# Optimization experiments

Measured on AMD Instinct MI355X. Metric: run time of the kernel, lower is better.

## Reference

```python
import jax, jax.numpy as jnp
import numpy as np

B_SZ = 4; SEQ = 2048; D_INPUT = 40; D_MODEL = 128; N_LAYERS = 4
D_STATE = 16; EXPAND = 2; D_INNER = D_MODEL * EXPAND
N_HEADS = 4; D_HEAD = D_MODEL // N_HEADS; MAX_LANDMARKS = 100
EPS_RMS = 1.1920929e-07  # torch nn.RMSNorm default eps = finfo(float32).eps
EPS_LN = 1e-5
A_FLOOR = 1e-4


def _rms(x, w):
    return x * jax.lax.rsqrt(jnp.mean(x * x, -1, keepdims=True) + EPS_RMS) * w


def _ln(x, w, b):
    m = jnp.mean(x, -1, keepdims=True)
    v = jnp.mean((x - m) ** 2, -1, keepdims=True)
    return (x - m) * jax.lax.rsqrt(v + EPS_LN) * w + b


def _mamba3_block(xin, Wi, Wx, Wdt, bdt, Alog, Bb, Cb, Bnw, Cnw, rf, Dv, Wo):
    # xin: (B,L,d_model)
    xz = xin @ Wi                       # (B,L,2*d_inner)
    xp, z = jnp.split(xz, 2, axis=-1)
    xp = jax.nn.silu(xp)
    sp = xp @ Wx                        # (B,L,2*d_state+2)
    B_raw = sp[..., :D_STATE]
    C_raw = sp[..., D_STATE:2 * D_STATE]
    dt_in = sp[..., -2:-1]
    lam_in = sp[..., -1:]
    Bm = _rms(B_raw + Bb, Bnw)
    Cm = _rms(C_raw + Cb, Cnw)
    dt = jax.nn.softplus(dt_in @ Wdt + bdt)   # (B,L,d_inner)
    lam = jax.nn.sigmoid(lam_in)              # (B,L,1)
    # data-dependent RoPE on B and C
    freqs = jax.nn.softplus(rf)                                  # (d_state//2,)
    ang = jnp.cumsum(jnp.mean(dt, -1, keepdims=True), axis=1) * freqs  # (B,L,ds/2)
    ca, sa = jnp.cos(ang), jnp.sin(ang)

    def rot(M):
        e, o = M[..., ::2], M[..., 1::2]
        return jnp.stack([e * ca - o * sa, e * sa + o * ca], -1).reshape(M.shape)

    Bm, Cm = rot(Bm), rot(Cm)
    A = jnp.minimum(-jnp.exp(Alog), -A_FLOOR)   # (d_inner,d_state)
    dte = dt[..., None]                          # (B,L,d_inner,1)
    dA = jnp.exp(A * dte)                        # (B,L,d_inner,d_state)
    Bx = Bm[:, :, None, :] * xp[..., None]       # (B,L,d_inner,d_state)
    Bx_prev = jnp.concatenate([jnp.zeros_like(Bx[:, :1]), Bx[:, :-1]], axis=1)
    lame = lam[..., None]                        # (B,L,1,1)
    u = (1.0 - lame) * dte * dA * Bx_prev + lame * dte * Bx
    u = u.at[:, 0].set(dte[:, 0] * Bx[:, 0])     # t==0 case: h = dt*B*x (no lambda)

    def step(h, inp):
        dA_t, u_t, C_t = inp
        h = dA_t * h + u_t
        return h, jnp.sum(h * C_t[:, None, :], -1)

    h0 = jnp.zeros((xin.shape[0], D_INNER, D_STATE), xin.dtype)
    _, ys = jax.lax.scan(step, h0, (jnp.swapaxes(dA, 0, 1), jnp.swapaxes(u, 0, 1), jnp.swapaxes(Cm, 0, 1)))
    y = jnp.swapaxes(ys, 0, 1)                   # (B,L,d_inner)
    y = y + xp * Dv
    y = y * jax.nn.silu(z)
    return y @ Wo


def _landmark_attn(mo, skip, hw, WQ, bQ, WK, bK, WV, bV, WO, bO):
    Bsz, L, Dm = skip.shape
    k = min(MAX_LANDMARKS, L)
    _, idx = jax.lax.top_k(hw, k)
    idx = jnp.sort(idx, axis=1)                            # (B,k)
    kv = jnp.take_along_axis(skip, idx[..., None], axis=1)  # (B,k,Dm)
    q = mo[:, -1:, :]                                       # (B,1,Dm)
    Q = (q @ WQ + bQ).reshape(Bsz, 1, N_HEADS, D_HEAD).transpose(0, 2, 1, 3)
    K = (kv @ WK + bK).reshape(Bsz, k, N_HEADS, D_HEAD).transpose(0, 2, 1, 3)
    V = (kv @ WV + bV).reshape(Bsz, k, N_HEADS, D_HEAD).transpose(0, 2, 1, 3)
    scores = jnp.einsum('bhqd,bhkd->bhqk', Q, K) * (D_HEAD ** -0.5)
    probs = jax.nn.softmax(scores, axis=-1)
    out = jnp.einsum('bhqk,bhkd->bhqd', probs, V).transpose(0, 2, 1, 3).reshape(Bsz, Dm)
    return out @ WO + bO


def setup_inputs() -> dict:
    key = jax.random.key(0)
    ks = iter(jax.random.split(key, 64))

    def nrm(shape, s=0.02):
        return jax.random.normal(next(ks), shape, jnp.float32) * s

    nl, ds, di, dm = N_LAYERS, D_STATE, D_INNER, D_MODEL
    inp = {}
    inp['x'] = jax.random.normal(next(ks), (B_SZ, SEQ, D_INPUT), jnp.float32)
    inp['hawkes_weights'] = jax.random.uniform(next(ks), (B_SZ, SEQ), jnp.float32)
    inp['emb_W'] = nrm((D_INPUT, dm)); inp['emb_b'] = jnp.zeros(dm, jnp.float32)
    inp['skip_W'] = nrm((D_INPUT, dm)); inp['skip_b'] = jnp.zeros(dm, jnp.float32)
    inp['in_proj_W'] = nrm((nl, dm, 2 * di))
    inp['x_proj_W'] = nrm((nl, di, 2 * ds + 2))
    inp['dt_proj_W'] = nrm((nl, 1, di), 1.0)
    inp['dt_proj_b'] = jnp.full((nl, di), -1.0, jnp.float32)
    inp['A_log'] = jnp.broadcast_to(jnp.log(jnp.arange(1, ds + 1, dtype=jnp.float32)), (nl, di, ds)) * jnp.ones((nl, di, ds), jnp.float32)
    inp['B_bias'] = jnp.ones((nl, ds), jnp.float32)
    inp['C_bias'] = jnp.ones((nl, ds), jnp.float32)
    inp['Bn_w'] = jnp.ones((nl, ds), jnp.float32)
    inp['Cn_w'] = jnp.ones((nl, ds), jnp.float32)
    inp['rope_freqs'] = nrm((nl, ds // 2), 0.01)
    inp['D_param'] = jnp.ones((nl, di), jnp.float32)
    inp['out_proj_W'] = nrm((nl, di, dm))
    inp['ln_w'] = jnp.ones((nl, dm), jnp.float32); inp['ln_b'] = jnp.zeros((nl, dm), jnp.float32)
    inp['fn_w'] = jnp.ones(dm, jnp.float32); inp['fn_b'] = jnp.zeros(dm, jnp.float32)
    for nm in ('Q', 'K', 'V', 'O'):
        inp['W' + nm] = nrm((dm, dm)); inp['b' + nm] = jnp.zeros(dm, jnp.float32)
    return inp


def reference(x, hawkes_weights, emb_W, emb_b, skip_W, skip_b, in_proj_W, x_proj_W,
              dt_proj_W, dt_proj_b, A_log, B_bias, C_bias, Bn_w, Cn_w, rope_freqs,
              D_param, out_proj_W, ln_w, ln_b, fn_w, fn_b, WQ, bQ, WK, bK, WV, bV, WO, bO):
    w = hawkes_weights[..., None]
    h = (x @ emb_W + emb_b) * w          # Hawkes-damped embedding for Mamba path
    skip = (x @ skip_W + skip_b) * w     # Hawkes skip for attention KV
    for i in range(N_LAYERS):
        h = h + _mamba3_block(_ln(h, ln_w[i], ln_b[i]), in_proj_W[i], x_proj_W[i],
                              dt_proj_W[i], dt_proj_b[i], A_log[i], B_bias[i], C_bias[i],
                              Bn_w[i], Cn_w[i], rope_freqs[i], D_param[i], out_proj_W[i])
    mo = _ln(h, fn_w, fn_b)
    return _landmark_attn(mo, skip, hawkes_weights, WQ, bQ, WK, bK, WV, bV, WO, bO)
```

## Files before the change

### kernel.cpp

```cpp
#include <hip/hip_runtime.h>
#include <hip/hip_fp16.h>
#include <math.h>

#define BSZ   4
#define SEQL  2048
#define DIN   40
#define DM    128
#define DI    256
#define DS    16
#define NL    4
#define NHEAD 4
#define DHEAD 32
#define KLM   100
#define NC    128
#define TC    16
#define NROWS 8
#define EROWS 16

__device__ __forceinline__ float rcp_(float x){ return __builtin_amdgcn_rcpf(x); }
__device__ __forceinline__ float sigmoidf_(float x){ return rcp_(1.0f + __expf(-x)); }
__device__ __forceinline__ float siluf_(float x){ return x*rcp_(1.0f + __expf(-x)); }
__device__ __forceinline__ float softplusf_(float x){ return fmaxf(x,0.0f) + __logf(1.0f + __expf(-fabsf(x))); }

__device__ __forceinline__ void load8(const float* p, float* r){
  const float4* q = (const float4*)p;
  float4 a=q[0], b=q[1];
  r[0]=a.x;r[1]=a.y;r[2]=a.z;r[3]=a.w; r[4]=b.x;r[5]=b.y;r[6]=b.z;r[7]=b.w;
}
__device__ __forceinline__ void store8(float* p, const float* r){
  float4* q = (float4*)p;
  q[0]=make_float4(r[0],r[1],r[2],r[3]);  q[1]=make_float4(r[4],r[5],r[6],r[7]);
}
__device__ __forceinline__ void load16(const float* p, float* r){
  load8(p, r); load8(p+8, r+8);
}
__device__ __forceinline__ void store16(float* p, const float* r){
  store8(p, r); store8(p+8, r+8);
}

__global__ __launch_bounds__(256) void topk_kernel(
    const float* __restrict__ hw, int* __restrict__ idxl_g)
{
  __shared__ int redcnt[2][4];
  __shared__ int eqc[8][4], gtc[8][4];

  const int b = blockIdx.x;
  const int t = threadIdx.x;
  const int lane = t & 63, w = t >> 6;

  const float* hwp = hw + (size_t)b*SEQL;
  unsigned vb[8];
  #pragma unroll
  for (int q=0;q<8;q++) vb[q] = __float_as_uint(hwp[q*256 + t]);

  unsigned kth = 0u;
  for (int bit=31; bit>=0; --bit){
    const unsigned cand = kth | (1u << bit);
    int c0 = 0;
    #pragma unroll
    for (int q=0;q<8;q++) c0 += __popcll(__ballot(vb[q] >= cand));
    const int par = bit & 1;
    if (lane == 0) redcnt[par][w] = c0;
    __syncthreads();
    const int tot = redcnt[par][0]+redcnt[par][1]+redcnt[par][2]+redcnt[par][3];
    if (tot >= KLM) kth = cand;
  }

  unsigned long long beq[8], bgt[8];
  #pragma unroll
  for (int q=0;q<8;q++){
    beq[q] = __ballot(vb[q] == kth);
    bgt[q] = __ballot(vb[q] >  kth);
  }
  if (lane == 0){
    #pragma unroll
    for (int q=0;q<8;q++){ eqc[q][w] = __popcll(beq[q]); gtc[q][w] = __popcll(bgt[q]); }
  }
  __syncthreads();
  {
    int gtTot = 0;
    #pragma unroll
    for (int q=0;q<8;q++) gtTot += gtc[q][0]+gtc[q][1]+gtc[q][2]+gtc[q][3];
    const int need_eq = KLM - gtTot;
    const unsigned long long lmask = (lane==0) ? 0ull : ((~0ull) >> (64-lane));
    int eqPfx = 0, gtPfx = 0;
    #pragma unroll
    for (int q=0;q<8;q++){
      int eqWP = 0, gtWP = 0;
      for (int w2=0; w2<w; ++w2){ eqWP += eqc[q][w2]; gtWP += gtc[q][w2]; }
      const int eqBefore = eqPfx + eqWP + __popcll(beq[q] & lmask);
      const int gtBefore = gtPfx + gtWP + __popcll(bgt[q] & lmask);
      if (vb[q] > kth){
        const int pos = gtBefore + min(eqBefore, need_eq);
        if (pos < KLM) idxl_g[b*KLM + pos] = q*256 + t;
      } else if (vb[q] == kth && eqBefore < need_eq){
        const int pos = gtBefore + eqBefore;
        if (pos < KLM) idxl_g[b*KLM + pos] = q*256 + t;
      }
      eqPfx += eqc[q][0]+eqc[q][1]+eqc[q][2]+eqc[q][3];
      gtPfx += gtc[q][0]+gtc[q][1]+gtc[q][2]+gtc[q][3];
    }
  }
}

__global__ __launch_bounds__(256) void embed_kernel(
    const float* __restrict__ x, const float* __restrict__ hw,
    const float* __restrict__ eW, const float* __restrict__ eb,
    const float* __restrict__ sW, const float* __restrict__ sb,
    float* __restrict__ hb, float* __restrict__ sk)
{
  __shared__ float xr[EROWS][DIN];
  const int t = threadIdx.x;
  const size_t R0 = (size_t)blockIdx.x * EROWS;
  for (int e=t; e<EROWS*DIN; e+=256) ((float*)xr)[e] = x[R0*DIN + e];
  __syncthreads();
  const int c = t & (DM-1), g = t >> 7;
  float ae[8], as[8];
  #pragma unroll
  for (int j=0;j<8;j++){ ae[j]=0.0f; as[j]=0.0f; }
  for (int k=0;k<DIN;k++){
    const float we  = eW[(size_t)k*DM + c];
    const float ws_ = sW[(size_t)k*DM + c];
    #pragma unroll
    for (int j=0;j<8;j++){
      const float xv = xr[g*8+j][k];
      ae[j] = fmaf(xv, we, ae[j]);
      as[j] = fmaf(xv, ws_, as[j]);
    }
  }
  const float ebv = eb[c], sbv = sb[c];
  #pragma unroll
  for (int j=0;j<8;j++){
    const size_t R = R0 + g*8 + j;
    const float w = hw[R];
    hb[R*DM + c] = (ae[j]+ebv)*w;
    sk[R*DM + c] = (as[j]+sbv)*w;
  }
}

__global__ __launch_bounds__(256) void pre_kernel(
    const float* __restrict__ hb,
    const float* __restrict__ Wi, const float* __restrict__ Wx,
    const float* __restrict__ Wdt, const float* __restrict__ bdt,
    const float* __restrict__ Bb, const float* __restrict__ Cb,
    const float* __restrict__ Bnw, const float* __restrict__ Cnw,
    const float* __restrict__ lnw, const float* __restrict__ lnb,
    __half* __restrict__ xph, __half* __restrict__ zsh,
    float* __restrict__ dtin, float* __restrict__ Shalf,
    float* __restrict__ Bmb, float* __restrict__ Cmb,
    float* __restrict__ lamb, float* __restrict__ mdtb)
{
  __shared__ float xin[NROWS][DM+4];
  __shared__ float xps[NROWS][DI+4];
  __shared__ float spl[NROWS][40];
  __shared__ float pr[NROWS][4];

  const int t = threadIdx.x;
  const size_t R0 = (size_t)blockIdx.x * NROWS;

  {
    const int r = t >> 5, j = t & 31;
    const float4 v = ((const float4*)(hb + (R0 + r)*DM))[j];
    float s = v.x+v.y+v.z+v.w;
    #pragma unroll
    for (int o=16;o>0;o>>=1) s += __shfl_xor(s,o,32);
    const float m = s*(1.0f/DM);
    const float dx=v.x-m, dy=v.y-m, dz=v.z-m, dw=v.w-m;
    float ss = dx*dx+dy*dy+dz*dz+dw*dw;
    #pragma unroll
    for (int o=16;o>0;o>>=1) ss += __shfl_xor(ss,o,32);
    const float inv = 1.0f/sqrtf(ss*(1.0f/DM) + 1e-5f);
    const int c = j*4;
    xin[r][c+0] = dx*inv*lnw[c+0] + lnb[c+0];
    xin[r][c+1] = dy*inv*lnw[c+1] + lnb[c+1];
    xin[r][c+2] = dz*inv*lnw[c+2] + lnb[c+2];
    xin[r][c+3] = dw*inv*lnw[c+3] + lnb[c+3];
  }
  __syncthreads();

  {
    float2 a[NROWS];
    #pragma unroll
    for (int r=0;r<NROWS;r++){ a[r].x=0.0f; a[r].y=0.0f; }
    for (int k=0;k<DM;k+=4){
      const float2 w0 = *(const float2*)&Wi[(size_t)(k+0)*(2*DI) + 2*t];
      const float2 w1 = *(const float2*)&Wi[(size_t)(k+1)*(2*DI) + 2*t];
      const float2 w2 = *(const float2*)&Wi[(size_t)(k+2)*(2*DI) + 2*t];
      const float2 w3 = *(const float2*)&Wi[(size_t)(k+3)*(2*DI) + 2*t];
      #pragma unroll
      for (int r=0;r<NROWS;r++){
        const float4 xv = *(const float4*)&xin[r][k];
        a[r].x = fmaf(xv.x,w0.x,a[r].x); a[r].y = fmaf(xv.x,w0.y,a[r].y);
        a[r].x = fmaf(xv.y,w1.x,a[r].x); a[r].y = fmaf(xv.y,w1.y,a[r].y);
        a[r].x = fmaf(xv.z,w2.x,a[r].x); a[r].y = fmaf(xv.z,w2.y,a[r].y);
        a[r].x = fmaf(xv.w,w3.x,a[r].x); a[r].y = fmaf(xv.w,w3.y,a[r].y);
      }
    }
    if (t < 128){
      #pragma unroll
      for (int r=0;r<NROWS;r++){
        const float sx = siluf_(a[r].x), sy = siluf_(a[r].y);
        xps[r][2*t] = sx; xps[r][2*t+1] = sy;
        *(__half2*)&xph[(R0+r)*DI + 2*t] =
            __halves2half2(__float2half_rn(sx), __float2half_rn(sy));
      }
    } else {
      const int zc = 2*t - 2*DI + DI;
      #pragma unroll
      for (int r=0;r<NROWS;r++){
        const float sx = siluf_(a[r].x), sy = siluf_(a[r].y);
        *(__half2*)&zsh[(R0+r)*DI + zc] =
            __halves2half2(__float2half_rn(sx), __float2half_rn(sy));
      }
    }
  }
  __syncthreads();

  if (t < 136){
    const int r = t & 7, op = t >> 3;
    float ax=0.0f, ay=0.0f;
    for (int k=0;k<DI;k+=4){
      const float4 xv = *(const float4*)&xps[r][k];
      const float2 w0 = *(const float2*)&Wx[(size_t)(k+0)*34 + 2*op];
      const float2 w1 = *(const float2*)&Wx[(size_t)(k+1)*34 + 2*op];
      const float2 w2 = *(const float2*)&Wx[(size_t)(k+2)*34 + 2*op];
      const float2 w3 = *(const float2*)&Wx[(size_t)(k+3)*34 + 2*op];
      ax = fmaf(xv.x,w0.x,ax); ay = fmaf(xv.x,w0.y,ay);
      ax = fmaf(xv.y,w1.x,ax); ay = fmaf(xv.y,w1.y,ay);
      ax = fmaf(xv.z,w2.x,ax); ay = fmaf(xv.z,w2.y,ay);
      ax = fmaf(xv.w,w3.x,ax); ay = fmaf(xv.w,w3.y,ay);
    }
    spl[r][2*op] = ax; spl[r][2*op+1] = ay;
  }
  __syncthreads();

  {
    const int half = t >> 7;
    const int r2 = (t >> 4) & 7, s2 = t & 15;
    const float* bias = half ? Cb : Bb;
    const float* wn   = half ? Cnw : Bnw;
    const float v = spl[r2][half*DS + s2] + bias[s2];
    float ss = v*v;
    #pragma unroll
    for (int o=8;o>0;o>>=1) ss += __shfl_xor(ss,o,16);
    const float inv = 1.0f/sqrtf(ss*(1.0f/DS) + 1.1920929e-07f);
    (half ? Cmb : Bmb)[(R0+r2)*DS + s2] = v*inv*wn[s2];
  }

  {
    const int lane = t & 63, w = t >> 6;
    const float wdt = Wdt[t], bdtv = bdt[t];
    float Sd = 0.0f;
    #pragma unroll
    for (int r=0;r<NROWS;r++){
      const float dval = softplusf_(fmaf(spl[r][32], wdt, bdtv));
      Sd += dval;
      float s = dval;
      #pragma unroll
      for (int o=32;o>0;o>>=1) s += __shfl_xor(s,o,64);
      if (lane==0) pr[r][w] = s;
    }
    Shalf[(size_t)blockIdx.x * DI + t] = Sd;
    if (t < NROWS){
      lamb[R0+t] = sigmoidf_(spl[t][33]);
      dtin[R0+t] = spl[t][32];
    }
  }
  __syncthreads();
  if (t < NROWS)
    mdtb[R0+t] = (pr[t][0]+pr[t][1]+pr[t][2]+pr[t][3])*(1.0f/DI);
}

__global__ __launch_bounds__(256) void cumsum_kernel(
    const float* __restrict__ mdt, double* __restrict__ csum_g)
{
  __shared__ double wsum[4];
  const int b = blockIdx.x, t = threadIdx.x;
  const int lane = t & 63, w = t >> 6;
  const float* p = mdt + (size_t)b*SEQL + (size_t)t*8;
  double v[8]; double s = 0.0;
  #pragma unroll
  for (int q=0;q<8;q++){ v[q] = (double)p[q]; s += v[q]; }
  double sc = s;
  #pragma unroll
  for (int o=1;o<64;o<<=1){
    const double nb = __shfl_up(sc, o, 64);
    if (lane >= o) sc += nb;
  }
  if (lane==63) wsum[w] = sc;
  __syncthreads();
  double woff = 0.0;
  for (int j=0;j<w;j++) woff += wsum[j];
  double run = woff + sc - s;
  double* dst = csum_g + (size_t)b*SEQL + (size_t)t*8;
  #pragma unroll
  for (int q=0;q<8;q++){ run += v[q]; dst[q] = run; }
}

__global__ __launch_bounds__(256) void csfill_kernel(
    const double* __restrict__ csum_g, const float* __restrict__ rf,
    float2* __restrict__ cst)
{
  __shared__ double fqs[8];
  const int t = threadIdx.x;
  if (t < 8){
    const double xfr = (double)rf[t];
    fqs[t] = fmax(xfr, 0.0) + log1p(exp(-fabs(xfr)));
  }
  __syncthreads();
  const int row = blockIdx.x*256 + t;
  const double ab = csum_g[row];
  const double TWO_PI = 6.283185307179586;
  const double INV2PI = 0.15915494309189535;
  float2 o8[8];
  #pragma unroll
  for (int f=0; f<8; f++){
    const double ang = ab * fqs[f];
    const double red = ang - floor(ang*INV2PI)*TWO_PI;
    float sa, ca;
    __sincosf((float)red, &sa, &ca);
    o8[f] = make_float2(ca, sa);
  }
  float4* dst = (float4*)&cst[(size_t)row*8];
  dst[0] = make_float4(o8[0].x,o8[0].y,o8[1].x,o8[1].y);
  dst[1] = make_float4(o8[2].x,o8[2].y,o8[3].x,o8[3].y);
  dst[2] = make_float4(o8[4].x,o8[4].y,o8[5].x,o8[5].y);
  dst[3] = make_float4(o8[6].x,o8[6].y,o8[7].x,o8[7].y);
}

__global__ __launch_bounds__(512) void scan1_kernel(
    const __half* __restrict__ xph, const float* __restrict__ dtin,
    const float* __restrict__ Wdt, const float* __restrict__ bdt,
    const float* __restrict__ Bmb, const float* __restrict__ lamb,
    const float2* __restrict__ cst,
    const float* __restrict__ Alog, float* __restrict__ hend)
{
  __shared__ float Bst[TC+1][DS];
  __shared__ float lst[TC];
  __shared__ float dsl[TC];
  __shared__ __half xpl[TC+1][DI+8];
  const int t = threadIdx.x;
  const int d  = t >> 1;
  const int s0 = (t & 1) * 8;
  const int c = blockIdx.x & (NC-1);
  const int b = blockIdx.x >> 7;
  const size_t bL = (size_t)b*SEQL;
  const int t0 = c*TC;
  const int id = blockIdx.x*256 + d;

  for (int e=t; e<(TC+1)*DS; e+=512){
    const int j = e >> 4, s = e & 15;
    const int trow = t0 - 1 + j;
    Bst[j][s] = (trow >= 0) ? Bmb[(bL + trow)*DS + s] : 0.0f;
  }
  for (int e=t; e<(TC+1)*DI; e+=512){
    const int j = e >> 8, dd = e & (DI-1);
    const int trow = t0 - 1 + j;
    xpl[j][dd] = (trow >= 0) ? xph[(bL + trow)*DI + dd] : __float2half_rn(0.0f);
  }
  if (t < TC){
    lst[t] = lamb[bL + t0 + t];
    dsl[t] = dtin[bL + t0 + t];
  }
  __syncthreads();
  if (t < 136){
    const int j = t >> 3, f = t & 7;
    const int trow = t0 - 1 + j;
    if (trow >= 0){
      const float2 cs = cst[((size_t)(bL + trow))*8 + f];
      const float e0 = Bst[j][2*f], o0 = Bst[j][2*f+1];
      Bst[j][2*f]   = e0*cs.x - o0*cs.y;
      Bst[j][2*f+1] = e0*cs.y + o0*cs.x;
    }
  }
  __syncthreads();

  float A[8];
  #pragma unroll
  for (int s=0;s<8;s++) A[s] = fminf(-__expf(Alog[d*DS + s0 + s]), -1e-4f);
  const float wdt = Wdt[d], bdtv = bdt[d];
  float h[8], Bprev[8];
  #pragma unroll
  for (int s=0;s<8;s++) h[s]=0.0f;
  float xpm1;
  int tstart;
  if (t0 > 0){
    #pragma unroll
    for (int s=0;s<8;s++) Bprev[s] = Bst[0][s0+s];
    xpm1 = __half2float(xpl[0][d]);
    tstart = 0;
  } else {
    const float dtv = softplusf_(fmaf(dsl[0], wdt, bdtv));
    const float xpv = __half2float(xpl[1][d]);
    #pragma unroll
    for (int s=0;s<8;s++){
      h[s] = dtv*(Bst[1][s0+s]*xpv);
      Bprev[s] = Bst[1][s0+s];
    }
    xpm1 = xpv;
    tstart = 1;
  }
  for (int j=tstart; j<TC; ++j){
    const float dtv = softplusf_(fmaf(dsl[j], wdt, bdtv));
    const float xpv = __half2float(xpl[j+1][d]);
    const float lamv = lst[j];
    const float dl = dtv*lamv;
    const float dml = dtv - dl;
    #pragma unroll
    for (int s=0;s<8;s++){
      const float a = __expf(A[s]*dtv);
      const float Bc = Bst[j+1][s0+s];
      const float u = fmaf(dml*a, Bprev[s]*xpm1, dl*(Bc*xpv));
      h[s] = fmaf(a, h[s], u);
      Bprev[s] = Bc;
    }
    xpm1 = xpv;
  }
  store8(hend + (size_t)id*DS + s0, h);
}

__global__ __launch_bounds__(128) void scan2_kernel(
    float* __restrict__ hend, const float* __restrict__ Shalf,
    const float* __restrict__ Alog)
{
  __shared__ float hS[NC][DS+1];
  __shared__ float pS[NC][DS+1];
  const int c = threadIdx.x;
  const int d = blockIdx.x & (DI-1);
  const int b = blockIdx.x >> 8;
  const float S = Shalf[(size_t)(b*(SEQL/NROWS) + 2*c)*DI + d]
                + Shalf[(size_t)(b*(SEQL/NROWS) + 2*c + 1)*DI + d];
  float P[DS], h[DS];
  #pragma unroll
  for (int s=0;s<DS;s++){
    const float A = fminf(-__expf(Alog[d*DS+s]), -1e-4f);
    P[s] = __expf(A*S);
  }
  load16(hend + (((size_t)(b*NC + c))*DI + d)*DS, h);
  #pragma unroll
  for (int s=0;s<DS;s++){ hS[c][s]=h[s]; pS[c][s]=P[s]; }
  __syncthreads();
  for (int off=1; off<NC; off<<=1){
    float hn[DS], pn[DS];
    const int src = c - off;
    if (src >= 0){
      #pragma unroll
      for (int s=0;s<DS;s++){ hn[s]=hS[src][s]; pn[s]=pS[src][s]; }
    }
    __syncthreads();
    if (src >= 0){
      #pragma unroll
      for (int s=0;s<DS;s++){
        h[s] = fmaf(P[s], hn[s], h[s]);
        P[s] *= pn[s];
        hS[c][s] = h[s]; pS[c][s] = P[s];
      }
    }
    __syncthreads();
  }
  float o[DS];
  if (c == 0){
    #pragma unroll
    for (int s=0;s<DS;s++) o[s] = 0.0f;
  } else {
    #pragma unroll
    for (int s=0;s<DS;s++) o[s] = hS[c-1][s];
  }
  store16(hend + (((size_t)(b*NC + c))*DI + d)*DS, o);
}

__global__ __launch_bounds__(512) void scan3post_kernel(
    const __half* __restrict__ xph, const float* __restrict__ dtin,
    const float* __restrict__ Wdt, const float* __restrict__ bdt,
    const float* __restrict__ Bmb, const float* __restrict__ Cmb,
    const float* __restrict__ lamb, const __half* __restrict__ zsh,
    const float2* __restrict__ cst,
    const float* __restrict__ Alog, const float* __restrict__ Dv,
    const float* __restrict__ Hin, const float* __restrict__ Wo,
    float* __restrict__ hb)
{
  __shared__ float Bst[TC+1][DS];
  __shared__ float Cst[TC][DS];
  __shared__ float lst[TC];
  __shared__ float dsl[TC];
  __shared__ __half xpl[TC+1][DI+8];
  __shared__ __half zsl[TC][DI+8];
  __shared__ float ys[TC][DI+4];
  const int t = threadIdx.x;
  const int d  = t >> 1;
  const int sh = t & 1;
  const int s0 = sh * 8;
  const int c = blockIdx.x & (NC-1);
  const int b = blockIdx.x >> 7;
  const size_t bL = (size_t)b*SEQL;
  const int t0 = c*TC;
  const int id = blockIdx.x*256 + d;

  for (int e=t; e<(TC+1)*DS; e+=512){
    const int j = e >> 4, s = e & 15;
    const int trow = t0 - 1 + j;
    Bst[j][s] = (trow >= 0) ? Bmb[(bL + trow)*DS + s] : 0.0f;
    if (j < TC) Cst[j][s] = Cmb[(bL + t0 + j)*DS + s];
  }
  for (int e=t; e<(TC+1)*DI; e+=512){
    const int j = e >> 8, dd = e & (DI-1);
    const int trow = t0 - 1 + j;
    xpl[j][dd] = (trow >= 0) ? xph[(bL + trow)*DI + dd] : __float2half_rn(0.0f);
    if (j < TC) zsl[j][dd] = zsh[(bL + t0 + j)*DI + dd];
  }
  if (t < TC){
    lst[t] = lamb[bL + t0 + t];
    dsl[t] = dtin[bL + t0 + t];
  }
  __syncthreads();
  if (t < 264){
    if (t < 136){
      const int j = t >> 3, f = t & 7;
      const int trow = t0 - 1 + j;
      if (trow >= 0){
        const float2 cs = cst[((size_t)(bL + trow))*8 + f];
        const float e0 = Bst[j][2*f], o0 = Bst[j][2*f+1];
        Bst[j][2*f]   = e0*cs.x - o0*cs.y;
        Bst[j][2*f+1] = e0*cs.y + o0*cs.x;
      }
    } else {
      const int e2 = t - 136;
      const int j = e2 >> 3, f = e2 & 7;
      const float2 cs = cst[((size_t)(bL + t0 + j))*8 + f];
      const float e0 = Cst[j][2*f], o0 = Cst[j][2*f+1];
      Cst[j][2*f]   = e0*cs.x - o0*cs.y;
      Cst[j][2*f+1] = e0*cs.y + o0*cs.x;
    }
  }
  __syncthreads();

  float A[8];
  #pragma unroll
  for (int s=0;s<8;s++) A[s] = fminf(-__expf(Alog[d*DS + s0 + s]), -1e-4f);
  const float wdt = Wdt[d], bdtv = bdt[d];
  const float dvp = Dv[d];
  float h[8], Bprev[8];
  load8(Hin + (size_t)id*DS + s0, h);
  float xpm1;
  int tstart;
  if (t0 > 0){
    #pragma unroll
    for (int s=0;s<8;s++) Bprev[s] = Bst[0][s0+s];
    xpm1 = __half2float(xpl[0][d]);
    tstart = 0;
  } else {
    const float dtv = softplusf_(fmaf(dsl[0], wdt, bdtv));
    const float xpv = __half2float(xpl[1][d]);
    float y = 0.0f;
    #pragma unroll
    for (int s=0;s<8;s++){
      h[s] = dtv*(Bst[1][s0+s]*xpv);
      y = fmaf(h[s], Cst[0][s0+s], y);
      Bprev[s] = Bst[1][s0+s];
    }
    const float ytot = y + __shfl_xor(y, 1, 64);
    if (sh == 0) ys[0][d] = (ytot + xpv*dvp)*__half2float(zsl[0][d]);
    xpm1 = xpv;
    tstart = 1;
  }
  for (int j=tstart; j<TC; ++j){
    const float dtv = softplusf_(fmaf(dsl[j], wdt, bdtv));
    const float xpv = __half2float(xpl[j+1][d]);
    const float lamv = lst[j];
    const float dl = dtv*lamv;
    const float dml = dtv - dl;
    float y = 0.0f;
    #pragma unroll
    for (int s=0;s<8;s++){
      const float a = __expf(A[s]*dtv);
      const float Bc = Bst[j+1][s0+s];
      const float u = fmaf(dml*a, Bprev[s]*xpm1, dl*(Bc*xpv));
      h[s] = fmaf(a, h[s], u);
      y = fmaf(h[s], Cst[j][s0+s], y);
      Bprev[s] = Bc;
    }
    const float ytot = y + __shfl_xor(y, 1, 64);
    if (sh == 0) ys[j][d] = (ytot + xpv*dvp)*__half2float(zsl[j][d]);
    xpm1 = xpv;
  }
  __syncthreads();

  {
    const int cg2  = t & 31;
    const int ks2  = (t >> 5) & 1;
    const int rg   = (t >> 6) & 3;
    const int ksHi = t >> 8;
    const int seg = ksHi*2 + ks2;
    const int k0 = seg*64;
    const int c0c = cg2*4;
    float acc[4][4];
    #pragma unroll
    for (int rr=0;rr<4;rr++){ acc[rr][0]=0.f; acc[rr][1]=0.f; acc[rr][2]=0.f; acc[rr][3]=0.f; }
    for (int k=k0; k<k0+64; k+=4){
      float4 yv[4];
      #pragma unroll
      for (int rr=0;rr<4;rr++) yv[rr] = *(const float4*)&ys[rg*4+rr][k];
      #pragma unroll
      for (int j=0;j<4;j++){
        const float4 wv = *(const float4*)&Wo[(size_t)(k+j)*DM + c0c];
        const float y0 = (j==0)?yv[0].x:(j==1)?yv[0].y:(j==2)?yv[0].z:yv[0].w;
        const float y1 = (j==0)?yv[1].x:(j==1)?yv[1].y:(j==2)?yv[1].z:yv[1].w;
        const float y2 = (j==0)?yv[2].x:(j==1)?yv[2].y:(j==2)?yv[2].z:yv[2].w;
        const float y3 = (j==0)?yv[3].x:(j==1)?yv[3].y:(j==2)?yv[3].z:yv[3].w;
        acc[0][0]=fmaf(y0,wv.x,acc[0][0]); acc[0][1]=fmaf(y0,wv.y,acc[0][1]);
        acc[0][2]=fmaf(y0,wv.z,acc[0][2]); acc[0][3]=fmaf(y0,wv.w,acc[0][3]);
        acc[1][0]=fmaf(y1,wv.x,acc[1][0]); acc[1][1]=fmaf(y1,wv.y,acc[1][1]);
        acc[1][2]=fmaf(y1,wv.z,acc[1][2]); acc[1][3]=fmaf(y1,wv.w,acc[1][3]);
        acc[2][0]=fmaf(y2,wv.x,acc[2][0]); acc[2][1]=fmaf(y2,wv.y,acc[2][1]);
        acc[2][2]=fmaf(y2,wv.z,acc[2][2]); acc[2][3]=fmaf(y2,wv.w,acc[2][3]);
        acc[3][0]=fmaf(y3,wv.x,acc[3][0]); acc[3][1]=fmaf(y3,wv.y,acc[3][1]);
        acc[3][2]=fmaf(y3,wv.z,acc[3][2]); acc[3][3]=fmaf(y3,wv.w,acc[3][3]);
      }
    }
    #pragma unroll
    for (int rr=0;rr<4;rr++){
      #pragma unroll
      for (int cc=0;cc<4;cc++) acc[rr][cc] += __shfl_down(acc[rr][cc], 32, 64);
    }
    float (*red)[132] = (float(*)[132])ys;
    __syncthreads();
    const int lane = t & 63;
    if (ksHi == 1 && lane < 32){
      #pragma unroll
      for (int rr=0;rr<4;rr++)
        *(float4*)&red[rg*4+rr][c0c] = make_float4(acc[rr][0],acc[rr][1],acc[rr][2],acc[rr][3]);
    }
    __syncthreads();
    if (ksHi == 0 && lane < 32){
      #pragma unroll
      for (int rr=0;rr<4;rr++){
        const float4 rv = *(const float4*)&red[rg*4+rr][c0c];
        const size_t row = bL + t0 + rg*4 + rr;
        float4 hv = *(const float4*)&hb[row*DM + c0c];
        hv.x += acc[rr][0] + rv.x; hv.y += acc[rr][1] + rv.y;
        hv.z += acc[rr][2] + rv.z; hv.w += acc[rr][3] + rv.w;
        *(float4*)&hb[row*DM + c0c] = hv;
      }
    }
  }
}

__global__ __launch_bounds__(256) void attnmid_kernel(
    const float* __restrict__ hb, const float* __restrict__ sk,
    const int* __restrict__ idxl_g,
    const float* __restrict__ fnw, const float* __restrict__ fnb,
    const float* __restrict__ WQ, const float* __restrict__ bQ,
    const float* __restrict__ WK, const float* __restrict__ bK,
    const float* __restrict__ WV, const float* __restrict__ bV,
    float* __restrict__ attnog)
{
  __shared__ float kv[KLM][DM+4];
  __shared__ float mo[DM];
  __shared__ float Qs[DHEAD];
  __shared__ float qk[DM];
  __shared__ float sc[KLM];
  __shared__ float pbar[DM];
  __shared__ float bterm_s;
  const int t = threadIdx.x;
  const int b = blockIdx.x >> 2, hh = blockIdx.x & 3;
  const int c0 = hh*DHEAD;

  if (t < 64){
    const float* hr = hb + ((size_t)b*SEQL + (SEQL-1))*DM;
    const float v0 = hr[t], v1 = hr[t+64];
    float s = v0+v1;
    #pragma unroll
    for (int o=32;o>0;o>>=1) s += __shfl_xor(s,o,64);
    const float m = s*(1.0f/DM);
    const float d0=v0-m, d1=v1-m;
    float ss = d0*d0 + d1*d1;
    #pragma unroll
    for (int o=32;o>0;o>>=1) ss += __shfl_xor(ss,o,64);
    const float inv = 1.0f/sqrtf(ss*(1.0f/DM) + 1e-5f);
    mo[t]    = d0*inv*fnw[t]    + fnb[t];
    mo[t+64] = d1*inv*fnw[t+64] + fnb[t+64];
  }
  for (int e=t; e<KLM*DM; e+=256){
    const int j = e >> 7, cc = e & (DM-1);
    kv[j][cc] = sk[((size_t)b*SEQL + idxl_g[b*KLM + j])*DM + cc];
  }
  __syncthreads();
  if (t < DHEAD){
    float a = bQ[c0+t];
    #pragma unroll 4
    for (int k=0;k<DM;k++) a = fmaf(mo[k], WQ[(size_t)k*DM + c0+t], a);
    Qs[t] = a;
  }
  __syncthreads();
  if (t < DM){
    float a = 0.0f;
    #pragma unroll
    for (int cc=0; cc<DHEAD; cc++) a = fmaf(WK[(size_t)t*DM + c0 + cc], Qs[cc], a);
    qk[t] = a;
  } else if (t == DM){
    float a = 0.0f;
    for (int cc=0; cc<DHEAD; cc++) a += bK[c0+cc]*Qs[cc];
    bterm_s = a;
  }
  __syncthreads();
  if (t < KLM){
    float a = bterm_s;
    for (int m=0;m<DM;m+=4){
      const float4 kvv = *(const float4*)&kv[t][m];
      const float4 qv  = *(const float4*)&qk[m];
      a = fmaf(kvv.x,qv.x,a); a = fmaf(kvv.y,qv.y,a);
      a = fmaf(kvv.z,qv.z,a); a = fmaf(kvv.w,qv.w,a);
    }
    sc[t] = a*0.17677669529663687f;
  }
  __syncthreads();
  if (t < 64){
    const int lane = t;
    const float v0 = (lane < KLM) ? sc[lane] : -3.0e38f;
    const float v1 = (lane+64 < KLM) ? sc[lane+64] : -3.0e38f;
    float mx = fmaxf(v0, v1);
    #pragma unroll
    for (int o2=32;o2>0;o2>>=1) mx = fmaxf(mx, __shfl_xor(mx,o2,64));
    const float e0 = (lane < KLM) ? __expf(v0-mx) : 0.0f;
    const float e1 = (lane+64 < KLM) ? __expf(v1-mx) : 0.0f;
    float sm = e0+e1;
    #pragma unroll
    for (int o2=32;o2>0;o2>>=1) sm += __shfl_xor(sm,o2,64);
    const float inv2 = rcp_(sm);
    if (lane < KLM) sc[lane] = e0*inv2;
    if (lane+64 < KLM) sc[lane+64] = e1*inv2;
  }
  __syncthreads();
  if (t < DM){
    float a = 0.0f;
    #pragma unroll 4
    for (int j=0;j<KLM;j++) a = fmaf(sc[j], kv[j][t], a);
    pbar[t] = a;
  }
  __syncthreads();
  if (t < DHEAD){
    const int cc = c0 + t;
    float a = bV[cc];
    #pragma unroll 4
    for (int m=0;m<DM;m++) a = fmaf(pbar[m], WV[(size_t)m*DM + cc], a);
    attnog[b*DM + cc] = a;
  }
}

__global__ __launch_bounds__(128) void attnout_kernel(
    const float* __restrict__ attnog, const float* __restrict__ WO,
    const float* __restrict__ bO, float* __restrict__ outp)
{
  __shared__ float ao[DM];
  const int b = blockIdx.x, t = threadIdx.x;
  ao[t] = attnog[b*DM + t];
  __syncthreads();
  float a = bO[t];
  #pragma unroll 4
  for (int c2=0;c2<DM;c2++) a = fmaf(ao[c2], WO[(size_t)c2*DM + t], a);
  outp[(size_t)b*DM + t] = a;
}

extern "C" void kernel_launch(void* const* d_in, const int* in_sizes, int n_in,
                              void* d_out, int out_size, void* d_ws, size_t ws_size,
                              hipStream_t stream)
{
  (void)in_sizes; (void)n_in; (void)out_size; (void)ws_size;
  const float* x    = (const float*)d_in[0];
  const float* hw   = (const float*)d_in[1];
  const float* embW = (const float*)d_in[2];
  const float* embB = (const float*)d_in[3];
  const float* skW  = (const float*)d_in[4];
  const float* skB  = (const float*)d_in[5];
  const float* inW  = (const float*)d_in[6];
  const float* xpW  = (const float*)d_in[7];
  const float* dtW  = (const float*)d_in[8];
  const float* dtB  = (const float*)d_in[9];
  const float* Alog = (const float*)d_in[10];
  const float* Bb   = (const float*)d_in[11];
  const float* Cb   = (const float*)d_in[12];
  const float* Bnw  = (const float*)d_in[13];
  const float* Cnw  = (const float*)d_in[14];
  const float* rf   = (const float*)d_in[15];
  const float* Dpar = (const float*)d_in[16];
  const float* outW = (const float*)d_in[17];
  const float* lnW  = (const float*)d_in[18];
  const float* lnB  = (const float*)d_in[19];
  const float* fnW  = (const float*)d_in[20];
  const float* fnB  = (const float*)d_in[21];
  const float* WQ = (const float*)d_in[22]; const float* bQ = (const float*)d_in[23];
  const float* WK = (const float*)d_in[24]; const float* bK = (const float*)d_in[25];
  const float* WV = (const float*)d_in[26]; const float* bV = (const float*)d_in[27];
  const float* WO = (const float*)d_in[28]; const float* bO = (const float*)d_in[29];

  float* ws = (float*)d_ws;
  size_t off = 0;
  float* hb    = ws + off; off += (size_t)BSZ*SEQL*DM;
  float* sk    = ws + off; off += (size_t)BSZ*SEQL*DM;
  __half* xph  = (__half*)(ws + off); off += (size_t)BSZ*SEQL*DI/2;
  __half* zsh  = (__half*)(ws + off); off += (size_t)BSZ*SEQL*DI/2;
  float* Bmb   = ws + off; off += (size_t)BSZ*SEQL*DS;
  float* Cmb   = ws + off; off += (size_t)BSZ*SEQL*DS;
  float* lamb  = ws + off; off += (size_t)BSZ*SEQL;
  float* mdtb  = ws + off; off += (size_t)BSZ*SEQL;
  float* dtin  = ws + off; off += (size_t)BSZ*SEQL;
  float* Shalf = ws + off; off += (size_t)BSZ*(SEQL/NROWS)*DI;
  float* hend  = ws + off; off += (size_t)BSZ*NC*DI*DS;
  float2* cst  = (float2*)(ws + off); off += (size_t)BSZ*SEQL*16;
  double* csum_g = (double*)(ws + off); off += (size_t)BSZ*SEQL*2;
  int* idxl_g  = (int*)(ws + off); off += (size_t)BSZ*KLM;
  float* attnog= ws + off; off += (size_t)BSZ*DM;

  topk_kernel<<<BSZ, 256, 0, stream>>>(hw, idxl_g);
  embed_kernel<<<BSZ*SEQL/EROWS, 256, 0, stream>>>(x, hw, embW, embB, skW, skB, hb, sk);

  for (int i=0;i<NL;i++){
    pre_kernel<<<BSZ*SEQL/NROWS, 256, 0, stream>>>(hb,
        inW + (size_t)i*DM*2*DI, xpW + (size_t)i*DI*34,
        dtW + (size_t)i*DI, dtB + (size_t)i*DI,
        Bb + i*DS, Cb + i*DS, Bnw + i*DS, Cnw + i*DS,
        lnW + i*DM, lnB + i*DM,
        xph, zsh, dtin, Shalf, Bmb, Cmb, lamb, mdtb);
    cumsum_kernel<<<BSZ, 256, 0, stream>>>(mdtb, csum_g);
    csfill_kernel<<<BSZ*SEQL/256, 256, 0, stream>>>(csum_g, rf + i*8, cst);
    scan1_kernel<<<BSZ*NC, 512, 0, stream>>>(xph, dtin,
        dtW + (size_t)i*DI, dtB + (size_t)i*DI,
        Bmb, lamb, cst, Alog + (size_t)i*DI*DS, hend);
    scan2_kernel<<<BSZ*DI, 128, 0, stream>>>(hend, Shalf, Alog + (size_t)i*DI*DS);
    scan3post_kernel<<<BSZ*NC, 512, 0, stream>>>(xph, dtin,
        dtW + (size_t)i*DI, dtB + (size_t)i*DI,
        Bmb, Cmb, lamb, zsh, cst,
        Alog + (size_t)i*DI*DS, Dpar + (size_t)i*DI, hend,
        outW + (size_t)i*DI*DM, hb);
  }

  attnmid_kernel<<<BSZ*NHEAD, 256, 0, stream>>>(hb, sk, idxl_g, fnW, fnB,
      WQ, bQ, WK, bK, WV, bV, attnog);
  attnout_kernel<<<BSZ, 128, 0, stream>>>(attnog, WO, bO, (float*)d_out);
}
```

Baseline: 506.7 us.

## Split pre and scan kernels across d_inner halves and add residual kernel

The pre kernel is launched with twice the blocks: each block computes either the x or the z half of the input projection, and the z blocks exit early. The scan1 and scan3post kernels split d_inner into two halves per chunk, with four threads per channel holding four states each. Each half writes a partial output projection to a new buffer, and a new resid_kernel adds both partials into the hidden state. The aim is more blocks, lower register pressure and better occupancy. In exchange it adds an extra kernel launch per layer, extra global traffic for the partial outputs, and a duplicated layernorm per row block in pre.

```diff
diff --git a/kernel.cpp b/kernel.cpp
--- a/kernel.cpp
+++ b/kernel.cpp
@@ -22,20 +22,18 @@
 __device__ __forceinline__ float siluf_(float x){ return x*rcp_(1.0f + __expf(-x)); }
 __device__ __forceinline__ float softplusf_(float x){ return fmaxf(x,0.0f) + __logf(1.0f + __expf(-fabsf(x))); }
 
-__device__ __forceinline__ void load8(const float* p, float* r){
-  const float4* q = (const float4*)p;
-  float4 a=q[0], b=q[1];
-  r[0]=a.x;r[1]=a.y;r[2]=a.z;r[3]=a.w; r[4]=b.x;r[5]=b.y;r[6]=b.z;r[7]=b.w;
-}
-__device__ __forceinline__ void store8(float* p, const float* r){
-  float4* q = (float4*)p;
-  q[0]=make_float4(r[0],r[1],r[2],r[3]);  q[1]=make_float4(r[4],r[5],r[6],r[7]);
+__device__ __forceinline__ void load4(const float* p, float* r){
+  const float4 a = *(const float4*)p;
+  r[0]=a.x; r[1]=a.y; r[2]=a.z; r[3]=a.w;
+}
+__device__ __forceinline__ void store4(float* p, const float* r){
+  *(float4*)p = make_float4(r[0],r[1],r[2],r[3]);
 }
 __device__ __forceinline__ void load16(const float* p, float* r){
-  load8(p, r); load8(p+8, r+8);
+  load4(p,r); load4(p+4,r+4); load4(p+8,r+8); load4(p+12,r+12);
 }
 __device__ __forceinline__ void store16(float* p, const float* r){
-  store8(p, r); store8(p+8, r+8);
+  store4(p,r); store4(p+4,r+4); store4(p+8,r+8); store4(p+12,r+12);
 }
 
 __global__ __launch_bounds__(256) void topk_kernel(
@@ -156,7 +154,9 @@
   __shared__ float pr[NROWS][4];
 
   const int t = threadIdx.x;
-  const size_t R0 = (size_t)blockIdx.x * NROWS;
+  const int rb = blockIdx.x >> 1;
+  const int typeB = blockIdx.x & 1;
+  const size_t R0 = (size_t)rb * NROWS;
 
   {
     const int r = t >> 5, j = t & 31;
@@ -179,39 +179,36 @@
   __syncthreads();
 
   {
-    float2 a[NROWS];
-    #pragma unroll
-    for (int r=0;r<NROWS;r++){ a[r].x=0.0f; a[r].y=0.0f; }
+    const int col = typeB*DI + t;
+    float acc[NROWS];
+    #pragma unroll
+    for (int r=0;r<NROWS;r++) acc[r] = 0.0f;
+    const float* Wc = Wi + col;
     for (int k=0;k<DM;k+=4){
-      const float2 w0 = *(const float2*)&Wi[(size_t)(k+0)*(2*DI) + 2*t];
-      const float2 w1 = *(const float2*)&Wi[(size_t)(k+1)*(2*DI) + 2*t];
-      const float2 w2 = *(const float2*)&Wi[(size_t)(k+2)*(2*DI) + 2*t];
-      const float2 w3 = *(const float2*)&Wi[(size_t)(k+3)*(2*DI) + 2*t];
+      const float w0 = Wc[(size_t)(k+0)*(2*DI)];
+      const float w1 = Wc[(size_t)(k+1)*(2*DI)];
+      const float w2 = Wc[(size_t)(k+2)*(2*DI)];
+      const float w3 = Wc[(size_t)(k+3)*(2*DI)];
       #pragma unroll
       for (int r=0;r<NROWS;r++){
         const float4 xv = *(const float4*)&xin[r][k];
-        a[r].x = fmaf(xv.x,w0.x,a[r].x); a[r].y = fmaf(xv.x,w0.y,a[r].y);
-        a[r].x = fmaf(xv.y,w1.x,a[r].x); a[r].y = fmaf(xv.y,w1.y,a[r].y);
-        a[r].x = fmaf(xv.z,w2.x,a[r].x); a[r].y = fmaf(xv.z,w2.y,a[r].y);
-        a[r].x = fmaf(xv.w,w3.x,a[r].x); a[r].y = fmaf(xv.w,w3.y,a[r].y);
+        float a = acc[r];
+        a = fmaf(xv.x,w0,a); a = fmaf(xv.y,w1,a);
+        a = fmaf(xv.z,w2,a); a = fmaf(xv.w,w3,a);
+        acc[r] = a;
       }
     }
-    if (t < 128){
+    if (typeB){
       #pragma unroll
-      for (int r=0;r<NROWS;r++){
-        const float sx = siluf_(a[r].x), sy = siluf_(a[r].y);
-        xps[r][2*t] = sx; xps[r][2*t+1] = sy;
-        *(__half2*)&xph[(R0+r)*DI + 2*t] =
-            __halves2half2(__float2half_rn(sx), __float2half_rn(sy));
-      }
-    } else {
-      const int zc = 2*t - 2*DI + DI;
-      #pragma unroll
-      for (int r=0;r<NROWS;r++){
-        const float sx = siluf_(a[r].x), sy = siluf_(a[r].y);
-        *(__half2*)&zsh[(R0+r)*DI + zc] =
-            __halves2half2(__float2half_rn(sx), __float2half_rn(sy));
-      }
+      for (int r=0;r<NROWS;r++)
+        zsh[(R0+r)*DI + t] = __float2half_rn(siluf_(acc[r]));
+      return;
+    }
+    #pragma unroll
+    for (int r=0;r<NROWS;r++){
+      const float sx = siluf_(acc[r]);
+      xps[r][t] = sx;
+      xph[(R0+r)*DI + t] = __float2half_rn(sx);
     }
   }
   __syncthreads();
@@ -260,7 +257,7 @@
       for (int o=32;o>0;o>>=1) s += __shfl_xor(s,o,64);
       if (lane==0) pr[r][w] = s;
     }
-    Shalf[(size_t)blockIdx.x * DI + t] = Sd;
+    Shalf[(size_t)rb * DI + t] = Sd;
     if (t < NROWS){
       lamb[R0+t] = sigmoidf_(spl[t][33]);
       dtin[R0+t] = spl[t][32];
@@ -338,25 +335,27 @@
   __shared__ float Bst[TC+1][DS];
   __shared__ float lst[TC];
   __shared__ float dsl[TC];
-  __shared__ __half xpl[TC+1][DI+8];
+  __shared__ __half xpl[TC+1][128+8];
   const int t = threadIdx.x;
-  const int d  = t >> 1;
-  const int s0 = (t & 1) * 8;
-  const int c = blockIdx.x & (NC-1);
-  const int b = blockIdx.x >> 7;
+  const int half = blockIdx.x & 1;
+  const int c = (blockIdx.x >> 1) & (NC-1);
+  const int b = blockIdx.x >> 8;
+  const int dl = t >> 2;
+  const int d  = half*128 + dl;
+  const int s0 = (t & 3)*4;
   const size_t bL = (size_t)b*SEQL;
   const int t0 = c*TC;
-  const int id = blockIdx.x*256 + d;
-
-  for (int e=t; e<(TC+1)*DS; e+=512){
-    const int j = e >> 4, s = e & 15;
+  const size_t idg = ((size_t)(b*NC + c))*DI + d;
+
+  if (t < 272){
+    const int j = t >> 4, s = t & 15;
     const int trow = t0 - 1 + j;
     Bst[j][s] = (trow >= 0) ? Bmb[(bL + trow)*DS + s] : 0.0f;
   }
-  for (int e=t; e<(TC+1)*DI; e+=512){
-    const int j = e >> 8, dd = e & (DI-1);
+  for (int e=t; e<(TC+1)*128; e+=512){
+    const int j = e >> 7, dd = e & 127;
     const int trow = t0 - 1 + j;
-    xpl[j][dd] = (trow >= 0) ? xph[(bL + trow)*DI + dd] : __float2half_rn(0.0f);
+    xpl[j][dd] = (trow >= 0) ? xph[(bL + trow)*DI + half*128 + dd] : __float2half_rn(0.0f);
   }
   if (t < TC){
     lst[t] = lamb[bL + t0 + t];
@@ -375,25 +374,25 @@
   }
   __syncthreads();
 
-  float A[8];
-  #pragma unroll
-  for (int s=0;s<8;s++) A[s] = fminf(-__expf(Alog[d*DS + s0 + s]), -1e-4f);
+  float A[4];
+  #pragma unroll
+  for (int s=0;s<4;s++) A[s] = fminf(-__expf(Alog[d*DS + s0 + s]), -1e-4f);
   const float wdt = Wdt[d], bdtv = bdt[d];
-  float h[8], Bprev[8];
-  #pragma unroll
-  for (int s=0;s<8;s++) h[s]=0.0f;
+  float h[4], Bprev[4];
+  #pragma unroll
+  for (int s=0;s<4;s++) h[s]=0.0f;
   float xpm1;
   int tstart;
   if (t0 > 0){
     #pragma unroll
-    for (int s=0;s<8;s++) Bprev[s] = Bst[0][s0+s];
-    xpm1 = __half2float(xpl[0][d]);
+    for (int s=0;s<4;s++) Bprev[s] = Bst[0][s0+s];
+    xpm1 = __half2float(xpl[0][dl]);
     tstart = 0;
   } else {
     const float dtv = softplusf_(fmaf(dsl[0], wdt, bdtv));
-    const float xpv = __half2float(xpl[1][d]);
-    #pragma unroll
-    for (int s=0;s<8;s++){
+    const float xpv = __half2float(xpl[1][dl]);
+    #pragma unroll
+    for (int s=0;s<4;s++){
       h[s] = dtv*(Bst[1][s0+s]*xpv);
       Bprev[s] = Bst[1][s0+s];
     }
@@ -402,21 +401,21 @@
   }
   for (int j=tstart; j<TC; ++j){
     const float dtv = softplusf_(fmaf(dsl[j], wdt, bdtv));
-    const float xpv = __half2float(xpl[j+1][d]);
+    const float xpv = __half2float(xpl[j+1][dl]);
     const float lamv = lst[j];
-    const float dl = dtv*lamv;
-    const float dml = dtv - dl;
-    #pragma unroll
-    for (int s=0;s<8;s++){
+    const float dl2 = dtv*lamv;
+    const float dml = dtv - dl2;
+    #pragma unroll
+    for (int s=0;s<4;s++){
       const float a = __expf(A[s]*dtv);
       const float Bc = Bst[j+1][s0+s];
-      const float u = fmaf(dml*a, Bprev[s]*xpm1, dl*(Bc*xpv));
+      const float u = fmaf(dml*a, Bprev[s]*xpm1, dl2*(Bc*xpv));
       h[s] = fmaf(a, h[s], u);
       Bprev[s] = Bc;
     }
     xpm1 = xpv;
   }
-  store8(hend + (size_t)id*DS + s0, h);
+  store4(hend + idg*DS + s0, h);
 }
 
 __global__ __launch_bounds__(128) void scan2_kernel(
@@ -477,36 +476,38 @@
     const float2* __restrict__ cst,
     const float* __restrict__ Alog, const float* __restrict__ Dv,
     const float* __restrict__ Hin, const float* __restrict__ Wo,
-    float* __restrict__ hb)
+    float* __restrict__ po)
 {
   __shared__ float Bst[TC+1][DS];
   __shared__ float Cst[TC][DS];
   __shared__ float lst[TC];
   __shared__ float dsl[TC];
-  __shared__ __half xpl[TC+1][DI+8];
-  __shared__ __half zsl[TC][DI+8];
-  __shared__ float ys[TC][DI+4];
+  __shared__ __half xpl[TC+1][128+8];
+  __shared__ __half zsl[TC][128+8];
+  __shared__ float ys[TC][128+4];
   const int t = threadIdx.x;
-  const int d  = t >> 1;
-  const int sh = t & 1;
-  const int s0 = sh * 8;
-  const int c = blockIdx.x & (NC-1);
-  const int b = blockIdx.x >> 7;
+  const int half = blockIdx.x & 1;
+  const int c = (blockIdx.x >> 1) & (NC-1);
+  const int b = blockIdx.x >> 8;
+  const int dl = t >> 2;
+  const int d  = half*128 + dl;
+  const int sq = t & 3;
+  const int s0 = sq*4;
   const size_t bL = (size_t)b*SEQL;
   const int t0 = c*TC;
-  const int id = blockIdx.x*256 + d;
-
-  for (int e=t; e<(TC+1)*DS; e+=512){
-    const int j = e >> 4, s = e & 15;
+  const size_t idg = ((size_t)(b*NC + c))*DI + d;
+
+  if (t < 272){
+    const int j = t >> 4, s = t & 15;
     const int trow = t0 - 1 + j;
     Bst[j][s] = (trow >= 0) ? Bmb[(bL + trow)*DS + s] : 0.0f;
     if (j < TC) Cst[j][s] = Cmb[(bL + t0 + j)*DS + s];
   }
-  for (int e=t; e<(TC+1)*DI; e+=512){
-    const int j = e >> 8, dd = e & (DI-1);
+  for (int e=t; e<(TC+1)*128; e+=512){
+    const int j = e >> 7, dd = e & 127;
     const int trow = t0 - 1 + j;
-    xpl[j][dd] = (trow >= 0) ? xph[(bL + trow)*DI + dd] : __float2half_rn(0.0f);
-    if (j < TC) zsl[j][dd] = zsh[(bL + t0 + j)*DI + dd];
+    xpl[j][dd] = (trow >= 0) ? xph[(bL + trow)*DI + half*128 + dd] : __float2half_rn(0.0f);
+    if (j < TC) zsl[j][dd] = zsh[(bL + t0 + j)*DI + half*128 + dd];
   }
   if (t < TC){
     lst[t] = lamb[bL + t0 + t];
@@ -534,115 +535,95 @@
   }
   __syncthreads();
 
-  float A[8];
-  #pragma unroll
-  for (int s=0;s<8;s++) A[s] = fminf(-__expf(Alog[d*DS + s0 + s]), -1e-4f);
+  float A[4];
+  #pragma unroll
+  for (int s=0;s<4;s++) A[s] = fminf(-__expf(Alog[d*DS + s0 + s]), -1e-4f);
   const float wdt = Wdt[d], bdtv = bdt[d];
   const float dvp = Dv[d];
-  float h[8], Bprev[8];
-  load8(Hin + (size_t)id*DS + s0, h);
+  float h[4], Bprev[4];
+  load4(Hin + idg*DS + s0, h);
   float xpm1;
   int tstart;
   if (t0 > 0){
     #pragma unroll
-    for (int s=0;s<8;s++) Bprev[s] = Bst[0][s0+s];
-    xpm1 = __half2float(xpl[0][d]);
+    for (int s=0;s<4;s++) Bprev[s] = Bst[0][s0+s];
+    xpm1 = __half2float(xpl[0][dl]);
     tstart = 0;
   } else {
     const float dtv = softplusf_(fmaf(dsl[0], wdt, bdtv));
-    const float xpv = __half2float(xpl[1][d]);
+    const float xpv = __half2float(xpl[1][dl]);
     float y = 0.0f;
     #pragma unroll
-    for (int s=0;s<8;s++){
+    for (int s=0;s<4;s++){
       h[s] = dtv*(Bst[1][s0+s]*xpv);
       y = fmaf(h[s], Cst[0][s0+s], y);
       Bprev[s] = Bst[1][s0+s];
     }
-    const float ytot = y + __shfl_xor(y, 1, 64);
-    if (sh == 0) ys[0][d] = (ytot + xpv*dvp)*__half2float(zsl[0][d]);
+    float ytot = y + __shfl_xor(y, 1, 64);
+    ytot += __shfl_xor(ytot, 2, 64);
+    if (sq == 0) ys[0][dl] = (ytot + xpv*dvp)*__half2float(zsl[0][dl]);
     xpm1 = xpv;
     tstart = 1;
   }
   for (int j=tstart; j<TC; ++j){
     const float dtv = softplusf_(fmaf(dsl[j], wdt, bdtv));
-    const float xpv = __half2float(xpl[j+1][d]);
+    const float xpv = __half2float(xpl[j+1][dl]);
     const float lamv = lst[j];
-    const float dl = dtv*lamv;
-    const float dml = dtv - dl;
+    const float dl2 = dtv*lamv;
+    const float dml = dtv - dl2;
     float y = 0.0f;
     #pragma unroll
-    for (int s=0;s<8;s++){
+    for (int s=0;s<4;s++){
       const float a = __expf(A[s]*dtv);
       const float Bc = Bst[j+1][s0+s];
-      const float u = fmaf(dml*a, Bprev[s]*xpm1, dl*(Bc*xpv));
+      const float u = fmaf(dml*a, Bprev[s]*xpm1, dl2*(Bc*xpv));
       h[s] = fmaf(a, h[s], u);
       y = fmaf(h[s], Cst[j][s0+s], y);
       Bprev[s] = Bc;
     }
-    const float ytot = y + __shfl_xor(y, 1, 64);
-    if (sh == 0) ys[j][d] = (ytot + xpv*dvp)*__half2float(zsl[j][d]);
+    float ytot = y + __shfl_xor(y, 1, 64);
+    ytot += __shfl_xor(ytot, 2, 64);
+    if (sq == 0) ys[j][dl] = (ytot + xpv*dvp)*__half2float(zsl[j][dl]);
     xpm1 = xpv;
   }
   __syncthreads();
 
   {
-    const int cg2  = t & 31;
-    const int ks2  = (t >> 5) & 1;
-    const int rg   = (t >> 6) & 3;
-    const int ksHi = t >> 8;
-    const int seg = ksHi*2 + ks2;
-    const int k0 = seg*64;
-    const int c0c = cg2*4;
-    float acc[4][4];
-    #pragma unroll
-    for (int rr=0;rr<4;rr++){ acc[rr][0]=0.f; acc[rr][1]=0.f; acc[rr][2]=0.f; acc[rr][3]=0.f; }
-    for (int k=k0; k<k0+64; k+=4){
-      float4 yv[4];
-      #pragma unroll
-      for (int rr=0;rr<4;rr++) yv[rr] = *(const float4*)&ys[rg*4+rr][k];
+    const int r  = t >> 5;
+    const int cq = t & 31;
+    const int c0c = cq*4;
+    float acc[4] = {0.0f,0.0f,0.0f,0.0f};
+    const float* Wh = Wo + (size_t)(half*128)*DM;
+    for (int kl=0; kl<128; kl+=4){
+      const float4 yv = *(const float4*)&ys[r][kl];
+      const float yy[4] = {yv.x, yv.y, yv.z, yv.w};
       #pragma unroll
       for (int j=0;j<4;j++){
-        const float4 wv = *(const float4*)&Wo[(size_t)(k+j)*DM + c0c];
-        const float y0 = (j==0)?yv[0].x:(j==1)?yv[0].y:(j==2)?yv[0].z:yv[0].w;
-        const float y1 = (j==0)?yv[1].x:(j==1)?yv[1].y:(j==2)?yv[1].z:yv[1].w;
-        const float y2 = (j==0)?yv[2].x:(j==1)?yv[2].y:(j==2)?yv[2].z:yv[2].w;
-        const float y3 = (j==0)?yv[3].x:(j==1)?yv[3].y:(j==2)?yv[3].z:yv[3].w;
-        acc[0][0]=fmaf(y0,wv.x,acc[0][0]); acc[0][1]=fmaf(y0,wv.y,acc[0][1]);
-        acc[0][2]=fmaf(y0,wv.z,acc[0][2]); acc[0][3]=fmaf(y0,wv.w,acc[0][3]);
-        acc[1][0]=fmaf(y1,wv.x,acc[1][0]); acc[1][1]=fmaf(y1,wv.y,acc[1][1]);
-        acc[1][2]=fmaf(y1,wv.z,acc[1][2]); acc[1][3]=fmaf(y1,wv.w,acc[1][3]);
-        acc[2][0]=fmaf(y2,wv.x,acc[2][0]); acc[2][1]=fmaf(y2,wv.y,acc[2][1]);
-        acc[2][2]=fmaf(y2,wv.z,acc[2][2]); acc[2][3]=fmaf(y2,wv.w,acc[2][3]);
-        acc[3][0]=fmaf(y3,wv.x,acc[3][0]); acc[3][1]=fmaf(y3,wv.y,acc[3][1]);
-        acc[3][2]=fmaf(y3,wv.z,acc[3][2]); acc[3][3]=fmaf(y3,wv.w,acc[3][3]);
+        const float4 wv = *(const float4*)&Wh[(size_t)(kl+j)*DM + c0c];
+        acc[0]=fmaf(yy[j],wv.x,acc[0]); acc[1]=fmaf(yy[j],wv.y,acc[1]);
+        acc[2]=fmaf(yy[j],wv.z,acc[2]); acc[3]=fmaf(yy[j],wv.w,acc[3]);
       }
     }
-    #pragma unroll
-    for (int rr=0;rr<4;rr++){
-      #pragma unroll
-      for (int cc=0;cc<4;cc++) acc[rr][cc] += __shfl_down(acc[rr][cc], 32, 64);
-    }
-    float (*red)[132] = (float(*)[132])ys;
-    __syncthreads();
-    const int lane = t & 63;
-    if (ksHi == 1 && lane < 32){
-      #pragma unroll
-      for (int rr=0;rr<4;rr++)
-        *(float4*)&red[rg*4+rr][c0c] = make_float4(acc[rr][0],acc[rr][1],acc[rr][2],acc[rr][3]);
-    }
-    __syncthreads();
-    if (ksHi == 0 && lane < 32){
-      #pragma unroll
-      for (int rr=0;rr<4;rr++){
-        const float4 rv = *(const float4*)&red[rg*4+rr][c0c];
-        const size_t row = bL + t0 + rg*4 + rr;
-        float4 hv = *(const float4*)&hb[row*DM + c0c];
-        hv.x += acc[rr][0] + rv.x; hv.y += acc[rr][1] + rv.y;
-        hv.z += acc[rr][2] + rv.z; hv.w += acc[rr][3] + rv.w;
-        *(float4*)&hb[row*DM + c0c] = hv;
-      }
-    }
-  }
+    const size_t row = bL + t0 + r;
+    *(float4*)&po[((size_t)half*BSZ*SEQL + row)*DM + c0c] =
+        make_float4(acc[0],acc[1],acc[2],acc[3]);
+  }
+}
+
+__global__ __launch_bounds__(256) void resid_kernel(
+    float* __restrict__ hb, const float* __restrict__ po)
+{
+  const size_t base = (size_t)blockIdx.x*2048 + (size_t)threadIdx.x*8;
+  const float* p0 = po + base;
+  const float* p1 = po + (size_t)BSZ*SEQL*DM + base;
+  float4 h0 = *(const float4*)&hb[base];
+  float4 h1 = *(const float4*)&hb[base+4];
+  const float4 a0 = *(const float4*)&p0[0], a1 = *(const float4*)&p0[4];
+  const float4 b0 = *(const float4*)&p1[0], b1 = *(const float4*)&p1[4];
+  h0.x += a0.x + b0.x; h0.y += a0.y + b0.y; h0.z += a0.z + b0.z; h0.w += a0.w + b0.w;
+  h1.x += a1.x + b1.x; h1.y += a1.y + b1.y; h1.z += a1.z + b1.z; h1.w += a1.w + b1.w;
+  *(float4*)&hb[base]   = h0;
+  *(float4*)&hb[base+4] = h1;
 }
 
 __global__ __launch_bounds__(256) void attnmid_kernel(
@@ -810,12 +791,13 @@
   double* csum_g = (double*)(ws + off); off += (size_t)BSZ*SEQL*2;
   int* idxl_g  = (int*)(ws + off); off += (size_t)BSZ*KLM;
   float* attnog= ws + off; off += (size_t)BSZ*DM;
+  float* po    = ws + off; off += (size_t)2*BSZ*SEQL*DM;
 
   topk_kernel<<<BSZ, 256, 0, stream>>>(hw, idxl_g);
   embed_kernel<<<BSZ*SEQL/EROWS, 256, 0, stream>>>(x, hw, embW, embB, skW, skB, hb, sk);
 
   for (int i=0;i<NL;i++){
-    pre_kernel<<<BSZ*SEQL/NROWS, 256, 0, stream>>>(hb,
+    pre_kernel<<<BSZ*SEQL/NROWS*2, 256, 0, stream>>>(hb,
         inW + (size_t)i*DM*2*DI, xpW + (size_t)i*DI*34,
         dtW + (size_t)i*DI, dtB + (size_t)i*DI,
         Bb + i*DS, Cb + i*DS, Bnw + i*DS, Cnw + i*DS,
@@ -823,15 +805,16 @@
         xph, zsh, dtin, Shalf, Bmb, Cmb, lamb, mdtb);
     cumsum_kernel<<<BSZ, 256, 0, stream>>>(mdtb, csum_g);
     csfill_kernel<<<BSZ*SEQL/256, 256, 0, stream>>>(csum_g, rf + i*8, cst);
-    scan1_kernel<<<BSZ*NC, 512, 0, stream>>>(xph, dtin,
+    scan1_kernel<<<BSZ*NC*2, 512, 0, stream>>>(xph, dtin,
         dtW + (size_t)i*DI, dtB + (size_t)i*DI,
         Bmb, lamb, cst, Alog + (size_t)i*DI*DS, hend);
     scan2_kernel<<<BSZ*DI, 128, 0, stream>>>(hend, Shalf, Alog + (size_t)i*DI*DS);
-    scan3post_kernel<<<BSZ*NC, 512, 0, stream>>>(xph, dtin,
+    scan3post_kernel<<<BSZ*NC*2, 512, 0, stream>>>(xph, dtin,
         dtW + (size_t)i*DI, dtB + (size_t)i*DI,
         Bmb, Cmb, lamb, zsh, cst,
         Alog + (size_t)i*DI*DS, Dpar + (size_t)i*DI, hend,
-        outW + (size_t)i*DI*DM, hb);
+        outW + (size_t)i*DI*DM, po);
+    resid_kernel<<<BSZ*SEQL/16, 256, 0, stream>>>(hb, po);
   }
 
   attnmid_kernel<<<BSZ*NHEAD, 256, 0, stream>>>(hb, sk, idxl_g, fnW, fnB,
```

New measurement: 682.1 us. +34.6%, slower.
